# Optimization experiments

Hardware: AMD Instinct MI355X
Metric: run time of the kernel (lower is better)

The kernel has to match this reference:

```python
import jax, jax.numpy as jnp
import numpy as np

# Dimensions: B=batch, T=decode len, S=source len, E=emb, H=rnn hidden, ENC=encoder size, V=vocab
B, T, S, E, H, ENC, V = 32, 64, 128, 256, 512, 512, 32000


def setup_inputs() -> dict:
    key = jax.random.key(0)
    ks = jax.random.split(key, 12)
    sc = lambda k, shape, s: jax.random.normal(k, shape, jnp.float32) * s
    return {
        "gold_tokens": jax.random.randint(ks[0], (B, T), 0, V),
        "enc_outputs": jax.random.normal(ks[1], (B, S, ENC), jnp.float32),
        "enc_lengths": jax.random.randint(ks[2], (B,), S // 2, S + 1),
        "h0": jnp.zeros((B, H), jnp.float32),
        "c0": jnp.zeros((B, H), jnp.float32),
        # learned parameters
        "embed_table": sc(ks[3], (V, E), 0.02),
        "W_ih": sc(ks[4], (4 * H, E), 0.05),   # torch LSTM gate order: i, f, g, o
        "W_hh": sc(ks[5], (4 * H, H), 0.05),
        "b_ih": jnp.zeros((4 * H,), jnp.float32),
        "b_hh": jnp.zeros((4 * H,), jnp.float32),
        "Wa": sc(ks[6], (H, ENC), 0.05),        # 'general' attention: score = q^T Wa k
        "Wc_w": sc(ks[7], (H, H + ENC), 0.05),  # Wc: Linear(rnn+enc -> ho=rnn)
        "Wc_b": jnp.zeros((H,), jnp.float32),
        "Wo_w": sc(ks[8], (V, H), 0.02),        # Wo: Linear(ho -> vocab)
        "Wo_b": jnp.zeros((V,), jnp.float32),
    }


def reference(gold_tokens, enc_outputs, enc_lengths, h0, c0, embed_table,
              W_ih, W_hh, b_ih, b_hh, Wa, Wc_w, Wc_b, Wo_w, Wo_b):
    S = enc_outputs.shape[1]
    # length mask for attention over encoder states
    mask = jnp.arange(S)[None, :] < enc_lengths[:, None]          # [B, S]
    # precompute Wa @ enc (invariant across decode steps)
    proj_enc = jnp.einsum('he,bse->bsh', Wa, enc_outputs)         # [B, S, H]
    embs = embed_table[gold_tokens]                               # [B, T, E] teacher forcing

    def step(carry, e_t):
        h, c = carry                                              # [B, H] each
        gates = e_t @ W_ih.T + b_ih + h @ W_hh.T + b_hh           # [B, 4H]
        i, f, g, o = jnp.split(gates, 4, axis=-1)
        c = jax.nn.sigmoid(f) * c + jax.nn.sigmoid(i) * jnp.tanh(g)
        h = jax.nn.sigmoid(o) * jnp.tanh(c)
        # general attention: score[b,s] = h[b] . (Wa enc[b,s])
        scores = jnp.einsum('bh,bsh->bs', h, proj_enc)
        scores = jnp.where(mask, scores, jnp.float32(-1e9))
        att = jax.nn.softmax(scores, axis=-1)                     # [B, S]
        ctx = jnp.einsum('bs,bse->be', att, enc_outputs)          # [B, ENC]
        ho = jnp.concatenate([h, ctx], axis=-1) @ Wc_w.T + Wc_b   # [B, H]
        logit = ho @ Wo_w.T + Wo_b                                # [B, V]
        return (h, c), logit

    (_, _), logits = jax.lax.scan(step, (h0, c0), jnp.swapaxes(embs, 0, 1))
    return jnp.swapaxes(logits, 0, 1)                             # [B, T, V]
```

## Files before the change

kernel.cpp:

```cpp
#include <hip/hip_runtime.h>

typedef unsigned short u16;
typedef unsigned int   u32;
typedef __attribute__((ext_vector_type(8))) __bf16 bf16x8;
typedef __attribute__((ext_vector_type(4))) float  f32x4;

#define B_   32
#define T_   64
#define S_   128
#define E_   256
#define H_   512
#define ENC_ 512
#define V_   32000

__device__ __forceinline__ float b2f(u16 u) {
  union { u32 i; float f; } v; v.i = ((u32)u) << 16; return v.f;
}
__device__ __forceinline__ u16 f2b(float f) {
  union { float f; u32 i; } v; v.f = f;
  u32 r = (v.i + 0x7fffu + ((v.i >> 16) & 1u)) >> 16;
  return (u16)r;
}
__device__ __forceinline__ float sigm(float x) { return 1.f / (1.f + __expf(-x)); }

__device__ __forceinline__ void async_ld16(const void* g, void* l) {
  __builtin_amdgcn_global_load_lds((const __attribute__((address_space(1))) u32*)g,
                                   (__attribute__((address_space(3))) u32*)l,
                                   16, 0, 0);
}

__global__ __launch_bounds__(256) void k_cvt(const float* __restrict__ src,
                                             u16* __restrict__ dst, int n4) {
  int i = blockIdx.x * 256 + threadIdx.x;
  if (i < n4) {
    float4 v = ((const float4*)src)[i];
    ushort4 o;
    o.x = f2b(v.x); o.y = f2b(v.y); o.z = f2b(v.z); o.w = f2b(v.w);
    ((ushort4*)dst)[i] = o;
  }
}

template <typename OUT_T>
__global__ __launch_bounds__(256) void gemm_bt(
    const u16* __restrict__ A, int lda,
    const u16* __restrict__ B, int ldb,
    OUT_T* __restrict__ C, int ldc, int K,
    const float* __restrict__ bias1, const float* __restrict__ bias2) {
  __shared__ __align__(16) u16 As[128 * 64];
  __shared__ __align__(16) u16 Bs[128 * 64];

  const int tid  = threadIdx.x;
  const int m0   = blockIdx.x * 128;
  const int n0   = blockIdx.y * 128;
  const int wave = tid >> 6, lane = tid & 63;
  const int mw = (wave >> 1) * 64, nw = (wave & 1) * 64;
  const int lr = lane & 15, lq = lane >> 4;

  f32x4 acc[4][4];
#pragma unroll
  for (int i = 0; i < 4; ++i)
#pragma unroll
    for (int j = 0; j < 4; ++j) acc[i][j] = (f32x4){0.f, 0.f, 0.f, 0.f};

  for (int k0 = 0; k0 < K; k0 += 64) {
#pragma unroll
    for (int it = 0; it < 4; ++it) {
      int chunk = it * 256 + tid;
      int row = chunk >> 3;
      int kc  = (chunk & 7) << 3;
      async_ld16(&A[(size_t)(m0 + row) * lda + k0 + kc], &As[chunk << 3]);
    }
#pragma unroll
    for (int it = 0; it < 4; ++it) {
      int chunk = it * 256 + tid;
      int row = chunk >> 3;
      int kc  = (chunk & 7) << 3;
      async_ld16(&B[(size_t)(n0 + row) * ldb + k0 + kc], &Bs[chunk << 3]);
    }
    __syncthreads();
#pragma unroll
    for (int kk = 0; kk < 2; ++kk) {
      bf16x8 af[4], bf[4];
#pragma unroll
      for (int i = 0; i < 4; ++i)
        af[i] = *(const bf16x8*)&As[(mw + i * 16 + lr) * 64 + kk * 32 + lq * 8];
#pragma unroll
      for (int j = 0; j < 4; ++j)
        bf[j] = *(const bf16x8*)&Bs[(nw + j * 16 + lr) * 64 + kk * 32 + lq * 8];
#pragma unroll
      for (int i = 0; i < 4; ++i)
#pragma unroll
        for (int j = 0; j < 4; ++j)
          acc[i][j] = __builtin_amdgcn_mfma_f32_16x16x32_bf16(af[i], bf[j], acc[i][j], 0, 0, 0);
    }
    __syncthreads();
  }

#pragma unroll
  for (int j = 0; j < 4; ++j) {
    int n = n0 + nw + j * 16 + lr;
    float bs = 0.f;
    if (bias1) bs += bias1[n];
    if (bias2) bs += bias2[n];
#pragma unroll
    for (int i = 0; i < 4; ++i) {
#pragma unroll
      for (int r = 0; r < 4; ++r) {
        int m = m0 + mw + i * 16 + lq * 4 + r;
        float v = acc[i][j][r] + bs;
        if constexpr (sizeof(OUT_T) == 2)
          C[(size_t)m * ldc + n] = (OUT_T)f2b(v);
        else
          C[(size_t)m * ldc + n] = v;
      }
    }
  }
}

__global__ __launch_bounds__(256) void k_embed(const int* __restrict__ toks,
                                               const float* __restrict__ table,
                                               u16* __restrict__ emb) {
  int id  = blockIdx.x * 256 + threadIdx.x;
  int row = id >> 6;
  int c4  = (id & 63) << 2;
  int tok = toks[row];
  float4 v = *(const float4*)&table[(size_t)tok * E_ + c4];
  ushort4 o;
  o.x = f2b(v.x); o.y = f2b(v.y); o.z = f2b(v.z); o.w = f2b(v.w);
  *(ushort4*)&emb[(size_t)row * E_ + c4] = o;
}

__global__ __launch_bounds__(256) void k_transpose(const float* __restrict__ Wa,
                                                   u16* __restrict__ WaT) {
  __shared__ float tle[32][33];
  int bx = blockIdx.x * 32;
  int by = blockIdx.y * 32;
  int tid = threadIdx.x;
  for (int i = tid; i < 1024; i += 256) {
    int r = i >> 5, c = i & 31;
    tle[r][c] = Wa[(size_t)(bx + r) * ENC_ + by + c];
  }
  __syncthreads();
  for (int i = tid; i < 1024; i += 256) {
    int r = i >> 5, c = i & 31;
    WaT[(size_t)(by + r) * H_ + bx + c] = f2b(tle[c][r]);
  }
}

__global__ __launch_bounds__(256) void k_lstm(
    const u16* __restrict__ Whh,
    const float* __restrict__ gp,
    const float* __restrict__ c0,
    u16* __restrict__ Hbuf,
    u16* __restrict__ hc,
    int* __restrict__ bar) {
  const int nblk = gridDim.x;
  const int blk  = blockIdx.x;
  const int tid  = threadIdx.x;
  const int wave = tid >> 6, lane = tid & 63;
  const int mi = wave >> 1, ni = wave & 1;
  const int lr = lane & 15, lq = lane >> 4;

  const int p    = ni * 16 + lr;
  const int grow = (p >> 3) * H_ + blk * 8 + (p & 7);
  bf16x8 bfr[16];
#pragma unroll
  for (int ks = 0; ks < 16; ++ks)
    bfr[ks] = *(const bf16x8*)&Whh[(size_t)grow * H_ + ks * 32 + lq * 8];

  const int pb = tid >> 3, pj = tid & 7;
  const int hidx = blk * 8 + pj;
  float c = c0[pb * H_ + hidx];

  __shared__ __align__(16) u16 Hs[32 * 512];
  __shared__ float G[32][33];

  const int am = mi * 16 + lr;

  float gpr[4];
#pragma unroll
  for (int r = 0; r < 4; ++r)
    gpr[r] = gp[(size_t)((mi * 16 + lq * 4 + r) * T_ + 0) * 2048 + grow];

#pragma unroll
  for (int it = 0; it < 8; ++it) {
    int chunk = it * 256 + tid;
    async_ld16(&Hbuf[chunk * 8], &Hs[chunk * 8]);
  }
  __syncthreads();

  for (int t = 0; t < T_; ++t) {
    f32x4 acc = (f32x4){0.f, 0.f, 0.f, 0.f};
#pragma unroll
    for (int ks = 0; ks < 16; ++ks) {
      bf16x8 a = *(const bf16x8*)&Hs[am * H_ + ks * 32 + lq * 8];
      acc = __builtin_amdgcn_mfma_f32_16x16x32_bf16(a, bfr[ks], acc, 0, 0, 0);
    }
#pragma unroll
    for (int r = 0; r < 4; ++r)
      G[mi * 16 + lq * 4 + r][p] = acc[r] + gpr[r];
    __syncthreads();
    float gi = G[pb][pj], gf = G[pb][8 + pj], gg = G[pb][16 + pj], go = G[pb][24 + pj];
    c = sigm(gf) * c + sigm(gi) * tanhf(gg);
    float h = sigm(go) * tanhf(c);
    u16 hb = f2b(h);
    u32 other = (u32)__shfl_xor((int)(u32)hb, 1);
    if (!(tid & 1)) {
      u32 pk = (u32)hb | (other << 16);
      __hip_atomic_store((u32*)&Hbuf[(size_t)(t + 1) * (B_ * H_) + pb * H_ + hidx], pk,
                         __ATOMIC_RELAXED, __HIP_MEMORY_SCOPE_AGENT);
      *(u32*)&hc[(size_t)(pb * T_ + t) * 1024 + hidx] = pk;
    }

    if (t < T_ - 1) {
#pragma unroll
      for (int r = 0; r < 4; ++r)
        gpr[r] = gp[(size_t)((mi * 16 + lq * 4 + r) * T_ + t + 1) * 2048 + grow];
      __syncthreads();
      if (tid == 0) {
        __hip_atomic_fetch_add(&bar[t], 1, __ATOMIC_RELAXED, __HIP_MEMORY_SCOPE_AGENT);
        while (__hip_atomic_load(&bar[t], __ATOMIC_RELAXED, __HIP_MEMORY_SCOPE_AGENT) < nblk) {
        }
      }
      __syncthreads();
      u32* hsrc = (u32*)&Hbuf[(size_t)(t + 1) * (B_ * H_)];
      u32 tmp[32];
#pragma unroll
      for (int it = 0; it < 32; ++it)
        tmp[it] = __hip_atomic_load(&hsrc[it * 256 + tid], __ATOMIC_RELAXED,
                                    __HIP_MEMORY_SCOPE_AGENT);
#pragma unroll
      for (int it = 0; it < 32; ++it)
        *(u32*)&Hs[(size_t)(it * 256 + tid) * 2] = tmp[it];
      __syncthreads();
    }
  }
}

__global__ __launch_bounds__(256) void k_attn(
    const u16* __restrict__ q,
    const u16* __restrict__ enc,
    const int* __restrict__ lens,
    u16* __restrict__ hc) {
  const int bt = blockIdx.x;
  const int b  = bt >> 6;
  const int tid = threadIdx.x;
  const int len = lens[b];

  __shared__ float qs[512];
  __shared__ float sc[128];
  __shared__ float red2[256];
  __shared__ float sred[2];

  for (int i = tid; i < 512; i += 256) qs[i] = b2f(q[(size_t)bt * 512 + i]);
  __syncthreads();

  {
    int s = tid & 127, half = tid >> 7;
    const u16* er = &enc[((size_t)b * S_ + s) * 512 + half * 256];
    const float* qb = &qs[half * 256];
    float a = 0.f;
#pragma unroll 4
    for (int k = 0; k < 256; k += 8) {
      uint4 raw = *(const uint4*)&er[k];
      u32 w0 = raw.x, w1 = raw.y, w2 = raw.z, w3 = raw.w;
      union { u32 i; float f; } lo, hi;
      lo.i = w0 << 16;          a += lo.f * qb[k + 0];
      hi.i = w0 & 0xffff0000u;  a += hi.f * qb[k + 1];
      lo.i = w1 << 16;          a += lo.f * qb[k + 2];
      hi.i = w1 & 0xffff0000u;  a += hi.f * qb[k + 3];
      lo.i = w2 << 16;          a += lo.f * qb[k + 4];
      hi.i = w2 & 0xffff0000u;  a += hi.f * qb[k + 5];
      lo.i = w3 << 16;          a += lo.f * qb[k + 6];
      hi.i = w3 & 0xffff0000u;  a += hi.f * qb[k + 7];
    }
    red2[tid] = a;
  }
  __syncthreads();
  if (tid < 128) {
    float v = red2[tid] + red2[tid + 128];
    sc[tid] = (tid < len) ? v : -1e30f;
  }
  __syncthreads();
  if (tid < 64) {
    float m = fmaxf(sc[tid], sc[tid + 64]);
#pragma unroll
    for (int o = 32; o > 0; o >>= 1) m = fmaxf(m, __shfl_down(m, o));
    if (tid == 0) sred[0] = m;
  }
  __syncthreads();
  float mx = sred[0];
  if (tid < 128) sc[tid] = __expf(sc[tid] - mx);
  __syncthreads();
  if (tid < 64) {
    float s2 = sc[tid] + sc[tid + 64];
#pragma unroll
    for (int o = 32; o > 0; o >>= 1) s2 += __shfl_down(s2, o);
    if (tid == 0) sred[1] = s2;
  }
  __syncthreads();
  float inv = 1.0f / sred[1];

  float a0 = 0.f, a1 = 0.f;
  for (int s = 0; s < S_; ++s) {
    float at = sc[s];
    const u16* er = &enc[((size_t)b * S_ + s) * 512];
    a0 += at * b2f(er[tid]);
    a1 += at * b2f(er[tid + 256]);
  }
  hc[(size_t)bt * 1024 + 512 + tid]       = f2b(a0 * inv);
  hc[(size_t)bt * 1024 + 512 + tid + 256] = f2b(a1 * inv);
}

extern "C" void kernel_launch(void* const* d_in, const int* in_sizes, int n_in,
                              void* d_out, int out_size, void* d_ws, size_t ws_size,
                              hipStream_t stream) {
  const int*   toks  = (const int*)d_in[0];
  const float* enc   = (const float*)d_in[1];
  const int*   lens  = (const int*)d_in[2];
  const float* h0    = (const float*)d_in[3];
  const float* c0    = (const float*)d_in[4];
  const float* table = (const float*)d_in[5];
  const float* W_ih  = (const float*)d_in[6];
  const float* W_hh  = (const float*)d_in[7];
  const float* b_ih  = (const float*)d_in[8];
  const float* b_hh  = (const float*)d_in[9];
  const float* Wa    = (const float*)d_in[10];
  const float* Wc_w  = (const float*)d_in[11];
  const float* Wc_b  = (const float*)d_in[12];
  const float* Wo_w  = (const float*)d_in[13];
  const float* Wo_b  = (const float*)d_in[14];
  float* out = (float*)d_out;

  char* ws = (char*)d_ws;
  size_t off = 0;
  auto alloc = [&](size_t bytes) {
    void* pp = ws + off;
    off += (bytes + 255) & ~(size_t)255;
    return pp;
  };
  int*   bar   = (int*)alloc(64 * sizeof(int));
  float* gp    = (float*)alloc((size_t)B_ * T_ * 2048 * 4);
  u16*   emb   = (u16*)alloc((size_t)B_ * T_ * E_ * 2);
  u16*   Hbuf  = (u16*)alloc((size_t)(T_ + 1) * B_ * H_ * 2);
  u16*   hc    = (u16*)alloc((size_t)B_ * T_ * 1024 * 2);
  u16*   q     = (u16*)alloc((size_t)B_ * T_ * ENC_ * 2);
  u16*   WaT   = (u16*)alloc((size_t)ENC_ * H_ * 2);
  u16*   ho    = (u16*)alloc((size_t)B_ * T_ * H_ * 2);
  u16*   Wihb  = (u16*)alloc((size_t)2048 * E_ * 2);
  u16*   Whhb  = (u16*)alloc((size_t)2048 * H_ * 2);
  u16*   Wcwb  = (u16*)alloc((size_t)H_ * 1024 * 2);
  u16*   Wowb  = (u16*)alloc((size_t)V_ * H_ * 2);
  u16*   encb  = (u16*)alloc((size_t)B_ * S_ * ENC_ * 2);
  (void)in_sizes; (void)n_in; (void)out_size; (void)ws_size;

  hipMemsetAsync(bar, 0, 64 * sizeof(int), stream);

  k_cvt<<<(2048 * E_ / 4 + 255) / 256, 256, 0, stream>>>(W_ih, Wihb, 2048 * E_ / 4);
  k_cvt<<<(2048 * H_ / 4 + 255) / 256, 256, 0, stream>>>(W_hh, Whhb, 2048 * H_ / 4);
  k_cvt<<<(H_ * 1024 / 4 + 255) / 256, 256, 0, stream>>>(Wc_w, Wcwb, H_ * 1024 / 4);
  k_cvt<<<(V_ * H_ / 4 + 255) / 256, 256, 0, stream>>>(Wo_w, Wowb, V_ * H_ / 4);
  k_cvt<<<(B_ * S_ * ENC_ / 4 + 255) / 256, 256, 0, stream>>>(enc, encb, B_ * S_ * ENC_ / 4);
  k_cvt<<<(B_ * H_ / 4 + 255) / 256, 256, 0, stream>>>(h0, Hbuf, B_ * H_ / 4);
  k_embed<<<512, 256, 0, stream>>>(toks, table, emb);
  gemm_bt<float><<<dim3(16, 16), 256, 0, stream>>>(emb, E_, Wihb, E_, gp, 2048, E_, b_ih, b_hh);
  k_transpose<<<dim3(16, 16), 256, 0, stream>>>(Wa, WaT);
  k_lstm<<<64, 256, 0, stream>>>(Whhb, gp, c0, Hbuf, hc, bar);
  gemm_bt<u16><<<dim3(16, 4), 256, 0, stream>>>(hc, 1024, WaT, H_, q, ENC_, H_, nullptr, nullptr);
  k_attn<<<B_ * T_, 256, 0, stream>>>(q, encb, lens, hc);
  gemm_bt<u16><<<dim3(16, 4), 256, 0, stream>>>(hc, 1024, Wcwb, 1024, ho, H_, 1024, Wc_b, nullptr);
  gemm_bt<float><<<dim3(16, 250), 256, 0, stream>>>(ho, H_, Wowb, H_, out, V_, H_, Wo_b, nullptr);
}
```

Baseline: 864.7 us.

## Replace atomic counter grid barrier with per-block flags and vectorized h loads

The per-step grid barrier in the persistent LSTM kernel used a single atomic counter that all 64 blocks incremented and spun on. It is replaced by per-(step, block) flags: each block stores its own flag, and one full wave polls all 64 flags at once with a wave-wide __all. The gate-projection prefetch now happens after the flag store. The hidden-state gather also changes from 32 relaxed atomic u32 loads per thread to 8 plain 16-byte loads, which cuts instruction count on the serial critical path. Both the flag signalling and the plain loads use relaxed ordering with no explicit fence, so cross-block visibility of h now depends on the hardware's memory behaviour.

```diff
diff --git a/kernel.cpp b/kernel.cpp
--- a/kernel.cpp
+++ b/kernel.cpp
@@ -153,8 +153,7 @@
     const float* __restrict__ c0,
     u16* __restrict__ Hbuf,
     u16* __restrict__ hc,
-    int* __restrict__ bar) {
-  const int nblk = gridDim.x;
+    int* __restrict__ flags) {
   const int blk  = blockIdx.x;
   const int tid  = threadIdx.x;
   const int wave = tid >> 6, lane = tid & 63;
@@ -213,25 +212,30 @@
     }
 
     if (t < T_ - 1) {
+      __syncthreads();
+      if (tid == 0)
+        __hip_atomic_store(&flags[t * 64 + blk], 1, __ATOMIC_RELAXED,
+                           __HIP_MEMORY_SCOPE_AGENT);
 #pragma unroll
       for (int r = 0; r < 4; ++r)
         gpr[r] = gp[(size_t)((mi * 16 + lq * 4 + r) * T_ + t + 1) * 2048 + grow];
-      __syncthreads();
-      if (tid == 0) {
-        __hip_atomic_fetch_add(&bar[t], 1, __ATOMIC_RELAXED, __HIP_MEMORY_SCOPE_AGENT);
-        while (__hip_atomic_load(&bar[t], __ATOMIC_RELAXED, __HIP_MEMORY_SCOPE_AGENT) < nblk) {
-        }
+      if (wave == 0) {
+        int f;
+        do {
+          f = __hip_atomic_load(&flags[t * 64 + lane], __ATOMIC_RELAXED,
+                                __HIP_MEMORY_SCOPE_AGENT);
+        } while (!__all(f != 0));
       }
       __syncthreads();
-      u32* hsrc = (u32*)&Hbuf[(size_t)(t + 1) * (B_ * H_)];
-      u32 tmp[32];
-#pragma unroll
-      for (int it = 0; it < 32; ++it)
-        tmp[it] = __hip_atomic_load(&hsrc[it * 256 + tid], __ATOMIC_RELAXED,
-                                    __HIP_MEMORY_SCOPE_AGENT);
-#pragma unroll
-      for (int it = 0; it < 32; ++it)
-        *(u32*)&Hs[(size_t)(it * 256 + tid) * 2] = tmp[it];
+      asm volatile("" ::: "memory");
+      const uint4* hsrc = (const uint4*)&Hbuf[(size_t)(t + 1) * (B_ * H_)];
+      uint4 tmp[8];
+#pragma unroll
+      for (int it = 0; it < 8; ++it)
+        tmp[it] = hsrc[it * 256 + tid];
+#pragma unroll
+      for (int it = 0; it < 8; ++it)
+        *(uint4*)&Hs[(size_t)(it * 256 + tid) * 8] = tmp[it];
       __syncthreads();
     }
   }
@@ -339,7 +343,7 @@
     off += (bytes + 255) & ~(size_t)255;
     return pp;
   };
-  int*   bar   = (int*)alloc(64 * sizeof(int));
+  int*   flags = (int*)alloc((size_t)T_ * 64 * sizeof(int));
   float* gp    = (float*)alloc((size_t)B_ * T_ * 2048 * 4);
   u16*   emb   = (u16*)alloc((size_t)B_ * T_ * E_ * 2);
   u16*   Hbuf  = (u16*)alloc((size_t)(T_ + 1) * B_ * H_ * 2);
@@ -354,7 +358,7 @@
   u16*   encb  = (u16*)alloc((size_t)B_ * S_ * ENC_ * 2);
   (void)in_sizes; (void)n_in; (void)out_size; (void)ws_size;
 
-  hipMemsetAsync(bar, 0, 64 * sizeof(int), stream);
+  hipMemsetAsync(flags, 0, (size_t)T_ * 64 * sizeof(int), stream);
 
   k_cvt<<<(2048 * E_ / 4 + 255) / 256, 256, 0, stream>>>(W_ih, Wihb, 2048 * E_ / 4);
   k_cvt<<<(2048 * H_ / 4 + 255) / 256, 256, 0, stream>>>(W_hh, Whhb, 2048 * H_ / 4);
@@ -365,7 +369,7 @@
   k_embed<<<512, 256, 0, stream>>>(toks, table, emb);
   gemm_bt<float><<<dim3(16, 16), 256, 0, stream>>>(emb, E_, Wihb, E_, gp, 2048, E_, b_ih, b_hh);
   k_transpose<<<dim3(16, 16), 256, 0, stream>>>(Wa, WaT);
-  k_lstm<<<64, 256, 0, stream>>>(Whhb, gp, c0, Hbuf, hc, bar);
+  k_lstm<<<64, 256, 0, stream>>>(Whhb, gp, c0, Hbuf, hc, flags);
   gemm_bt<u16><<<dim3(16, 4), 256, 0, stream>>>(hc, 1024, WaT, H_, q, ENC_, H_, nullptr, nullptr);
   k_attn<<<B_ * T_, 256, 0, stream>>>(q, encb, lens, hc);
   gemm_bt<u16><<<dim3(16, 4), 256, 0, stream>>>(hc, 1024, Wcwb, 1024, ho, H_, 1024, Wc_b, nullptr);
```

New measurement: 871.6 us. About the same (+0.8%).
